# Performance work log

Measured on AMD Instinct MI355X. Metric: run time of the kernel, lower is better.

Reference implementation:

```python
import jax, jax.numpy as jnp
import numpy as np

COUNT_BINS = 8
BOUND = 3.0
MIN_BIN_WIDTH = 1e-3
MIN_BIN_HEIGHT = 1e-3
MIN_DERIVATIVE = 1e-3
EPS = 1e-6


def _made_masks(D, H1, H2, M):
    indeg = np.arange(1, D + 1)                     # input degrees 1..D
    h1 = np.arange(H1) % (D - 1) + 1                # hidden degrees in [1, D-1]
    h2 = np.arange(H2) % (D - 1) + 1
    outdeg = np.tile(indeg, M)                      # (M*D,), reshape-compatible with (M, D)
    m1 = (h1[:, None] >= indeg[None, :]).astype(np.float32)   # (H1, D)
    m2 = (h2[:, None] >= h1[None, :]).astype(np.float32)      # (H2, H1)
    m3 = (outdeg[:, None] > h2[None, :]).astype(np.float32)   # (M*D, H2)
    return jnp.asarray(m1), jnp.asarray(m2), jnp.asarray(m3)


def _rq_spline_forward(x, w, h, d):
    # x: (B, D); w, h: (B, D, K) simplex weights; d: (B, D, K-1) softplus'd interior derivatives
    K = w.shape[-1]
    left, right = -BOUND, BOUND

    widths = MIN_BIN_WIDTH + (1.0 - MIN_BIN_WIDTH * K) * w
    heights = MIN_BIN_HEIGHT + (1.0 - MIN_BIN_HEIGHT * K) * h
    derivs = MIN_DERIVATIVE + d
    ones = jnp.ones_like(derivs[..., :1])
    derivs = jnp.concatenate([ones, derivs, ones], -1)          # (B, D, K+1), boundary slope 1

    cw = jnp.cumsum(widths, -1)
    edge_l = jnp.full_like(cw[..., :1], left)
    edge_r = jnp.full_like(cw[..., :1], right)
    cumw = jnp.concatenate([edge_l, left + (right - left) * cw[..., :-1], edge_r], -1)  # (B, D, K+1)
    widths = cumw[..., 1:] - cumw[..., :-1]
    ch = jnp.cumsum(heights, -1)
    cumh = jnp.concatenate([edge_l, left + (right - left) * ch[..., :-1], edge_r], -1)
    heights = cumh[..., 1:] - cumh[..., :-1]

    inside = (x >= left) & (x <= right)
    xc = jnp.clip(x, left, right)
    # pyro: bin_idx = sum(x >= cumwidths + eps) - 1
    idx = jnp.sum((xc[..., None] >= (cumw + EPS)).astype(jnp.int32), -1) - 1
    idx = jnp.clip(idx, 0, K - 1)                               # (B, D)

    def g(t):
        return jnp.take_along_axis(t, idx[..., None], axis=-1)[..., 0]

    x_k, w_k = g(cumw), g(widths)
    y_k, h_k = g(cumh), g(heights)
    delta = h_k / w_k
    d_k, d_k1 = g(derivs), g(derivs[..., 1:])

    theta = (xc - x_k) / w_k
    tt = theta * (1.0 - theta)
    num = h_k * (delta * theta ** 2 + d_k * tt)
    den = delta + (d_k + d_k1 - 2.0 * delta) * tt
    y = y_k + num / den
    dnum = delta ** 2 * (d_k1 * theta ** 2 + 2.0 * delta * tt + d_k * (1.0 - theta) ** 2)
    ld = jnp.log(dnum) - 2.0 * jnp.log(den)
    return jnp.where(inside, y, x), jnp.where(inside, ld, jnp.zeros_like(ld))


def _forward(x, W1, b1, W2, b2, W3, b3):
    B, D = x.shape
    H1, H2 = W1.shape[0], W2.shape[0]
    K = COUNT_BINS
    M = 3 * K - 1
    m1, m2, m3 = _made_masks(D, H1, H2, M)
    h1 = jax.nn.relu(x @ (W1 * m1).T + b1)
    h2 = jax.nn.relu(h1 @ (W2 * m2).T + b2)
    p = (h2 @ (W3 * m3).T + b3).reshape(B, M, D)                # (B, 3K-1, D)
    w = jax.nn.softmax(jnp.swapaxes(p[:, :K, :], 1, 2), axis=-1)          # (B, D, K)
    hgt = jax.nn.softmax(jnp.swapaxes(p[:, K:2 * K, :], 1, 2), axis=-1)   # (B, D, K)
    d = jax.nn.softplus(jnp.swapaxes(p[:, 2 * K:, :], 1, 2))              # (B, D, K-1)
    z, ld = _rq_spline_forward(x, w, hgt, d)
    return z, ld.sum(-1)


def setup_inputs() -> dict:
    key = jax.random.key(0)
    ks = jax.random.split(key, 7)
    B, D, H1, H2 = 32768, 64, 64, 32
    M = 3 * COUNT_BINS - 1
    s1, s2, s3 = 1.0 / np.sqrt(D), 1.0 / np.sqrt(H1), 1.0 / np.sqrt(H2)
    return {
        "x": jax.random.normal(ks[0], (B, D), jnp.float32),
        "W1": jax.random.uniform(ks[1], (H1, D), jnp.float32, -s1, s1),
        "b1": jax.random.uniform(ks[2], (H1,), jnp.float32, -s1, s1),
        "W2": jax.random.uniform(ks[3], (H2, H1), jnp.float32, -s2, s2),
        "b2": jax.random.uniform(ks[4], (H2,), jnp.float32, -s2, s2),
        "W3": jax.random.uniform(ks[5], (M * D, H2), jnp.float32, -s3, s3),
        "b3": jax.random.uniform(ks[6], (M * D,), jnp.float32, -s3, s3),
    }


def reference(x, W1, b1, W2, b2, W3, b3):
    return _forward(x, W1, b1, W2, b2, W3, b3)
```

## Files before the change

### kernel.cpp

```cpp
#include <hip/hip_runtime.h>

#define NM 23

typedef short short8 __attribute__((ext_vector_type(8)));
typedef float f32x4 __attribute__((ext_vector_type(4)));

#define LOG2E 1.44269504088896340736f

__device__ __forceinline__ float softplus_f(float v) {
  return fmaxf(v, 0.f) + __logf(1.f + __expf(-fabsf(v)));
}

__device__ __forceinline__ float fastrcp(float v) {
  return __builtin_amdgcn_rcpf(v);
}

__device__ __forceinline__ unsigned short bf16_rne(float x) {
  unsigned u = __float_as_uint(x);
  u += 0x7FFFu + ((u >> 16) & 1u);
  return (unsigned short)(u >> 16);
}

__global__ __launch_bounds__(256) void prep_kernel(
    const float* __restrict__ W1, const float* __restrict__ W2,
    const float* __restrict__ W3,
    unsigned short* __restrict__ B1hi,
    unsigned short* __restrict__ B2hi,
    unsigned short* __restrict__ B3hi) {
  const int idx = blockIdx.x * 256 + threadIdx.x;
  const int j = idx & 7, lane = (idx >> 3) & 63;
  const int col = lane & 15, quad = lane >> 4;

  if (idx < 4096) {
    const int rest = idx >> 9, kt = rest & 1, nt = rest >> 1;
    const int k = kt * 32 + quad * 8 + j;
    const int n = nt * 16 + col;
    const float v = ((n % 63) >= k) ? W1[n * 64 + k] : 0.f;
    B1hi[idx] = bf16_rne(v);
  }
  if (idx < 2048) {
    const int rest = idx >> 9, kt = rest & 1, nt = rest >> 1;
    const int k = kt * 32 + quad * 8 + j;
    const int n = nt * 16 + col;
    const float v = ((k % 63) <= n) ? W2[n * 64 + k] : 0.f;
    B2hi[idx] = bf16_rne(v);
  }
  if (idx < 92 * 64 * 8) {
    const int nt = idx >> 9;
    const int n = nt * 16 + col;
    const int d = n & 63;
    const int m = n >> 6;
    const int k = quad * 8 + j;
    float v = (k < d) ? W3[(size_t)n * 32 + k] : 0.f;
    if (m < 16) v *= LOG2E;
    B3hi[idx] = bf16_rne(v);
  }
}

__device__ __forceinline__ short8 cvt_hi(const float* src) {
  const f32x4 a0 = *reinterpret_cast<const f32x4*>(src);
  const f32x4 a1 = *reinterpret_cast<const f32x4*>(src + 4);
  const float af[8] = {a0.x, a0.y, a0.z, a0.w, a1.x, a1.y, a1.z, a1.w};
  short8 hi;
  #pragma unroll
  for (int j = 0; j < 8; ++j) hi[j] = (short)bf16_rne(af[j]);
  return hi;
}

__global__ __launch_bounds__(256, 4) void fused_kernel(
    const float* __restrict__ x,
    const unsigned short* __restrict__ B1hi,
    const float* __restrict__ b1,
    const unsigned short* __restrict__ B2hi,
    const float* __restrict__ b2,
    const unsigned short* __restrict__ B3hi,
    const float* __restrict__ b3,
    float* __restrict__ out, int B) {
  __shared__ float h1s[16][68];
  __shared__ float h2s[16][68];
  __shared__ float b3s[64 * NM];
  __shared__ float ldp[4][16];

  const int t = threadIdx.x;
  const int b0 = blockIdx.x * 16;

  for (int idx = t; idx < 64 * NM; idx += 256) {
    const int dl = idx / NM, m = idx - dl * NM;
    const float s = (m < 16) ? LOG2E : 1.f;
    b3s[idx] = b3[m * 64 + dl] * s;
  }
  __syncthreads();

  const int lane = t & 63;
  const int wv   = __builtin_amdgcn_readfirstlane(t >> 6);
  const int col  = lane & 15;
  const int quad = lane >> 4;

  {
    const int nt1 = wv;
    const float* xrow = x + (size_t)(b0 + col) * 64;
    short8 ah[2];
    #pragma unroll
    for (int kt = 0; kt < 2; ++kt)
      ah[kt] = cvt_hi(xrow + kt * 32 + quad * 8);

    const float bv = b1[nt1 * 16 + col];
    f32x4 acc = {bv, bv, bv, bv};
    #pragma unroll
    for (int kt = 0; kt < 2; ++kt) {
      const size_t off = ((size_t)(nt1 * 2 + kt) * 64 + lane) * 8;
      const short8 bh = *reinterpret_cast<const short8*>(B1hi + off);
      acc = __builtin_amdgcn_mfma_f32_16x16x32_bf16(ah[kt], bh, acc, 0, 0, 0);
    }
    #pragma unroll
    for (int reg = 0; reg < 4; ++reg)
      h1s[quad * 4 + reg][nt1 * 16 + col] = fmaxf(acc[reg], 0.f);
  }
  __syncthreads();

  if (wv < 2) {
    const int nt2 = wv;
    short8 ah[2];
    #pragma unroll
    for (int kt = 0; kt < 2; ++kt)
      ah[kt] = cvt_hi(&h1s[col][kt * 32 + quad * 8]);

    const float bv = b2[nt2 * 16 + col];
    f32x4 acc = {bv, bv, bv, bv};
    #pragma unroll
    for (int kt = 0; kt < 2; ++kt) {
      const size_t off = ((size_t)(nt2 * 2 + kt) * 64 + lane) * 8;
      const short8 bh = *reinterpret_cast<const short8*>(B2hi + off);
      acc = __builtin_amdgcn_mfma_f32_16x16x32_bf16(ah[kt], bh, acc, 0, 0, 0);
    }
    #pragma unroll
    for (int reg = 0; reg < 4; ++reg)
      h2s[quad * 4 + reg][nt2 * 16 + col] = fmaxf(acc[reg], 0.f);
  }
  __syncthreads();

  const int dc = wv;
  const int row0 = quad * 4;
  const int d = dc * 16 + col;

  const short8 ah = cvt_hi(&h2s[col][quad * 8]);

  float xvv[4];
  #pragma unroll
  for (int reg = 0; reg < 4; ++reg)
    xvv[reg] = x[(size_t)(b0 + row0 + reg) * 64 + d];

  __syncthreads();

  float ldr[4] = {0.f, 0.f, 0.f, 0.f};
  const float WSC = 1.0f - 1e-3f * 8.0f;

  float xcv[4], fidx[4], xkv[4], wkv[4], ykv[4], hkv[4];

  {
    f32x4 acc[8];
    #pragma unroll
    for (int m = 0; m < 8; ++m) {
      const float bv = b3s[d * NM + m];
      acc[m] = (f32x4){bv, bv, bv, bv};
    }
    #pragma unroll
    for (int m = 0; m < 8; ++m) {
      const size_t off = ((size_t)(4 * m + dc) * 64 + lane) * 8;
      const short8 bh = *reinterpret_cast<const short8*>(B3hi + off);
      acc[m] = __builtin_amdgcn_mfma_f32_16x16x32_bf16(ah, bh, acc[m], 0, 0, 0);
    }
    #pragma unroll
    for (int reg = 0; reg < 4; ++reg) {
      float ew[8], sw = 0.f;
      #pragma unroll
      for (int k = 0; k < 8; ++k) { ew[k] = exp2f(acc[k][reg]); sw += ew[k]; }
      const float scale = 6.f * WSC * fastrcp(sw);
      float cumw[9];
      cumw[0] = -3.f;
      float prefE = 0.f;
      #pragma unroll
      for (int k = 0; k < 7; ++k) {
        prefE += ew[k];
        const float Ck = -3.f + 6e-3f * (float)(k + 1);
        cumw[k + 1] = fmaf(prefE, scale, Ck);
      }
      cumw[8] = 3.f;

      const float xv = xvv[reg];
      const float xc = fminf(fmaxf(xv, -3.f), 3.f);
      float fi = 0.f, xk = cumw[0], xk1 = cumw[1];
      #pragma unroll
      for (int k = 1; k < 8; ++k) {
        const bool s = xc >= cumw[k] + 1e-6f;
        xk  = s ? cumw[k]     : xk;
        xk1 = s ? cumw[k + 1] : xk1;
        fi  = s ? (float)k    : fi;
      }
      xcv[reg] = xc; fidx[reg] = fi; xkv[reg] = xk; wkv[reg] = xk1 - xk;
    }
  }

  {
    f32x4 acc[8];
    #pragma unroll
    for (int m = 0; m < 8; ++m) {
      const float bv = b3s[d * NM + (8 + m)];
      acc[m] = (f32x4){bv, bv, bv, bv};
    }
    #pragma unroll
    for (int m = 0; m < 8; ++m) {
      const size_t off = ((size_t)(4 * (8 + m) + dc) * 64 + lane) * 8;
      const short8 bh = *reinterpret_cast<const short8*>(B3hi + off);
      acc[m] = __builtin_amdgcn_mfma_f32_16x16x32_bf16(ah, bh, acc[m], 0, 0, 0);
    }
    #pragma unroll
    for (int reg = 0; reg < 4; ++reg) {
      float eh[8], sh = 0.f;
      #pragma unroll
      for (int k = 0; k < 8; ++k) { eh[k] = exp2f(acc[k][reg]); sh += eh[k]; }
      const float scale = 6.f * WSC * fastrcp(sh);
      float cumh[9];
      cumh[0] = -3.f;
      float prefE = 0.f;
      #pragma unroll
      for (int k = 0; k < 7; ++k) {
        prefE += eh[k];
        const float Ck = -3.f + 6e-3f * (float)(k + 1);
        cumh[k + 1] = fmaf(prefE, scale, Ck);
      }
      cumh[8] = 3.f;

      float yk = cumh[0], yk1 = cumh[1];
      #pragma unroll
      for (int k = 1; k < 8; ++k) {
        const bool s = fidx[reg] >= (float)k;
        yk  = s ? cumh[k]     : yk;
        yk1 = s ? cumh[k + 1] : yk1;
      }
      ykv[reg] = yk; hkv[reg] = yk1 - yk;
    }
  }

  {
    f32x4 acc[7];
    #pragma unroll
    for (int m = 0; m < 7; ++m) {
      const float bv = b3s[d * NM + (16 + m)];
      acc[m] = (f32x4){bv, bv, bv, bv};
    }
    #pragma unroll
    for (int m = 0; m < 7; ++m) {
      const size_t off = ((size_t)(4 * (16 + m) + dc) * 64 + lane) * 8;
      const short8 bh = *reinterpret_cast<const short8*>(B3hi + off);
      acc[m] = __builtin_amdgcn_mfma_f32_16x16x32_bf16(ah, bh, acc[m], 0, 0, 0);
    }
    #pragma unroll
    for (int reg = 0; reg < 4; ++reg) {
      float p[7];
      #pragma unroll
      for (int k = 0; k < 7; ++k) p[k] = acc[k][reg];
      const float fi = fidx[reg];

      float pa = p[0], pb = p[0];
      #pragma unroll
      for (int k = 2; k < 8; ++k) pa = (fi >= (float)k) ? p[k - 1] : pa;
      #pragma unroll
      for (int k = 1; k < 7; ++k) pb = (fi >= (float)k) ? p[k] : pb;
      const float spa = 1e-3f + softplus_f(pa);
      const float spb = 1e-3f + softplus_f(pb);
      const float dk  = (fi >= 0.5f) ? spa : 1.f;
      const float dk1 = (fi >= 6.5f) ? 1.f : spb;

      const float xc = xcv[reg], xk = xkv[reg], wk = wkv[reg];
      const float yk = ykv[reg], hk = hkv[reg];
      const float invwk = fastrcp(wk);
      const float delta = hk * invwk;
      const float theta = (xc - xk) * invwk;
      const float omt = 1.f - theta;
      const float tt = theta * omt;
      const float th2 = theta * theta;
      const float num = hk * (delta * th2 + dk * tt);
      const float den = delta + (dk + dk1 - 2.f * delta) * tt;
      const float rden = fastrcp(den);
      const float yv = yk + num * rden;
      const float dnum =
          delta * delta * (dk1 * th2 + 2.f * delta * tt + dk * omt * omt);
      const float ldv = __logf(dnum * rden * rden);

      const float xv = xvv[reg];
      const bool inside = (xv >= -3.f) && (xv <= 3.f);
      h2s[row0 + reg][d] = inside ? yv : xv;
      ldr[reg] += inside ? ldv : 0.f;
    }
  }

  #pragma unroll
  for (int mask = 1; mask <= 8; mask <<= 1) {
    #pragma unroll
    for (int reg = 0; reg < 4; ++reg)
      ldr[reg] += __shfl_xor(ldr[reg], mask, 64);
  }
  if (col == 0) {
    #pragma unroll
    for (int reg = 0; reg < 4; ++reg)
      ldp[dc][row0 + reg] = ldr[reg];
  }

  __syncthreads();

  if (t < 16)
    out[(size_t)B * 64 + b0 + t] =
        (ldp[0][t] + ldp[1][t]) + (ldp[2][t] + ldp[3][t]);

  {
    const int rr = t >> 4, c4 = (t & 15) * 4;
    const float4 v = make_float4(h2s[rr][c4 + 0], h2s[rr][c4 + 1],
                                 h2s[rr][c4 + 2], h2s[rr][c4 + 3]);
    *reinterpret_cast<float4*>(out + (size_t)(b0 + rr) * 64 + c4) = v;
  }
}

extern "C" void kernel_launch(void* const* d_in, const int* in_sizes, int n_in,
                              void* d_out, int out_size, void* d_ws, size_t ws_size,
                              hipStream_t stream) {
  const float* x  = (const float*)d_in[0];
  const float* W1 = (const float*)d_in[1];
  const float* b1 = (const float*)d_in[2];
  const float* W2 = (const float*)d_in[3];
  const float* b2 = (const float*)d_in[4];
  const float* W3 = (const float*)d_in[5];
  const float* b3 = (const float*)d_in[6];
  float* out = (float*)d_out;
  char* ws   = (char*)d_ws;

  unsigned short* B1hi = (unsigned short*)(ws);
  unsigned short* B2hi = (unsigned short*)(ws + 8192);
  unsigned short* B3hi = (unsigned short*)(ws + 16384);

  const int B = in_sizes[0] / 64;

  prep_kernel<<<184, 256, 0, stream>>>(W1, W2, W3, B1hi, B2hi, B3hi);

  fused_kernel<<<B / 16, 256, 0, stream>>>(
      x, B1hi, b1, B2hi, b2, B3hi, b3, out, B);
}
```

Measured before the change: 103.5 us.

## Recompute MLP hidden layers per wave to eliminate block barriers

Each wave now computes all of layers 1 and 2 redundantly into its own shared-memory slice instead of splitting the tiles across waves. This removes the block-wide barriers between the layers and before the spline stage, and lets each wave write its own output columns directly. In exchange, the layer-1 and layer-2 MFMA work and weight loads are duplicated four times and shared memory per block grows.

```diff
diff --git a/kernel.cpp b/kernel.cpp
--- a/kernel.cpp
+++ b/kernel.cpp
@@ -76,8 +76,7 @@
     const unsigned short* __restrict__ B3hi,
     const float* __restrict__ b3,
     float* __restrict__ out, int B) {
-  __shared__ float h1s[16][68];
-  __shared__ float h2s[16][68];
+  __shared__ float slc[4][16][68];
   __shared__ float b3s[64 * NM];
   __shared__ float ldp[4][16];
 
@@ -95,62 +94,63 @@
   const int wv   = __builtin_amdgcn_readfirstlane(t >> 6);
   const int col  = lane & 15;
   const int quad = lane >> 4;
-
-  {
-    const int nt1 = wv;
+  float (*my)[68] = slc[wv];
+
+  {
     const float* xrow = x + (size_t)(b0 + col) * 64;
     short8 ah[2];
     #pragma unroll
     for (int kt = 0; kt < 2; ++kt)
       ah[kt] = cvt_hi(xrow + kt * 32 + quad * 8);
 
-    const float bv = b1[nt1 * 16 + col];
-    f32x4 acc = {bv, bv, bv, bv};
-    #pragma unroll
-    for (int kt = 0; kt < 2; ++kt) {
-      const size_t off = ((size_t)(nt1 * 2 + kt) * 64 + lane) * 8;
-      const short8 bh = *reinterpret_cast<const short8*>(B1hi + off);
-      acc = __builtin_amdgcn_mfma_f32_16x16x32_bf16(ah[kt], bh, acc, 0, 0, 0);
-    }
-    #pragma unroll
-    for (int reg = 0; reg < 4; ++reg)
-      h1s[quad * 4 + reg][nt1 * 16 + col] = fmaxf(acc[reg], 0.f);
-  }
-  __syncthreads();
-
-  if (wv < 2) {
-    const int nt2 = wv;
+    #pragma unroll
+    for (int nt = 0; nt < 4; ++nt) {
+      const float bv = b1[nt * 16 + col];
+      f32x4 acc = {bv, bv, bv, bv};
+      #pragma unroll
+      for (int kt = 0; kt < 2; ++kt) {
+        const size_t off = ((size_t)(nt * 2 + kt) * 64 + lane) * 8;
+        const short8 bh = *reinterpret_cast<const short8*>(B1hi + off);
+        acc = __builtin_amdgcn_mfma_f32_16x16x32_bf16(ah[kt], bh, acc, 0, 0, 0);
+      }
+      #pragma unroll
+      for (int reg = 0; reg < 4; ++reg)
+        my[quad * 4 + reg][nt * 16 + col] = fmaxf(acc[reg], 0.f);
+    }
+  }
+
+  {
     short8 ah[2];
     #pragma unroll
     for (int kt = 0; kt < 2; ++kt)
-      ah[kt] = cvt_hi(&h1s[col][kt * 32 + quad * 8]);
-
-    const float bv = b2[nt2 * 16 + col];
-    f32x4 acc = {bv, bv, bv, bv};
-    #pragma unroll
-    for (int kt = 0; kt < 2; ++kt) {
-      const size_t off = ((size_t)(nt2 * 2 + kt) * 64 + lane) * 8;
-      const short8 bh = *reinterpret_cast<const short8*>(B2hi + off);
-      acc = __builtin_amdgcn_mfma_f32_16x16x32_bf16(ah[kt], bh, acc, 0, 0, 0);
-    }
-    #pragma unroll
-    for (int reg = 0; reg < 4; ++reg)
-      h2s[quad * 4 + reg][nt2 * 16 + col] = fmaxf(acc[reg], 0.f);
-  }
-  __syncthreads();
+      ah[kt] = cvt_hi(&my[col][kt * 32 + quad * 8]);
+
+    #pragma unroll
+    for (int nt = 0; nt < 2; ++nt) {
+      const float bv = b2[nt * 16 + col];
+      f32x4 acc = {bv, bv, bv, bv};
+      #pragma unroll
+      for (int kt = 0; kt < 2; ++kt) {
+        const size_t off = ((size_t)(nt * 2 + kt) * 64 + lane) * 8;
+        const short8 bh = *reinterpret_cast<const short8*>(B2hi + off);
+        acc = __builtin_amdgcn_mfma_f32_16x16x32_bf16(ah[kt], bh, acc, 0, 0, 0);
+      }
+      #pragma unroll
+      for (int reg = 0; reg < 4; ++reg)
+        my[quad * 4 + reg][nt * 16 + col] = fmaxf(acc[reg], 0.f);
+    }
+  }
 
   const int dc = wv;
   const int row0 = quad * 4;
   const int d = dc * 16 + col;
 
-  const short8 ah = cvt_hi(&h2s[col][quad * 8]);
+  const short8 ah = cvt_hi(&my[col][quad * 8]);
 
   float xvv[4];
   #pragma unroll
   for (int reg = 0; reg < 4; ++reg)
     xvv[reg] = x[(size_t)(b0 + row0 + reg) * 64 + d];
-
-  __syncthreads();
 
   float ldr[4] = {0.f, 0.f, 0.f, 0.f};
   const float WSC = 1.0f - 1e-3f * 8.0f;
@@ -290,7 +290,7 @@
 
       const float xv = xvv[reg];
       const bool inside = (xv >= -3.f) && (xv <= 3.f);
-      h2s[row0 + reg][d] = inside ? yv : xv;
+      my[row0 + reg][d] = inside ? yv : xv;
       ldr[reg] += inside ? ldv : 0.f;
     }
   }
@@ -305,6 +305,16 @@
     #pragma unroll
     for (int reg = 0; reg < 4; ++reg)
       ldp[dc][row0 + reg] = ldr[reg];
+  }
+
+  {
+    const int rr = lane >> 2, ci = (lane & 3) * 4;
+    const float4 v = make_float4(my[rr][dc * 16 + ci + 0],
+                                 my[rr][dc * 16 + ci + 1],
+                                 my[rr][dc * 16 + ci + 2],
+                                 my[rr][dc * 16 + ci + 3]);
+    *reinterpret_cast<float4*>(
+        out + (size_t)(b0 + rr) * 64 + dc * 16 + ci) = v;
   }
 
   __syncthreads();
@@ -312,13 +322,6 @@
   if (t < 16)
     out[(size_t)B * 64 + b0 + t] =
         (ldp[0][t] + ldp[1][t]) + (ldp[2][t] + ldp[3][t]);
-
-  {
-    const int rr = t >> 4, c4 = (t & 15) * 4;
-    const float4 v = make_float4(h2s[rr][c4 + 0], h2s[rr][c4 + 1],
-                                 h2s[rr][c4 + 2], h2s[rr][c4 + 3]);
-    *reinterpret_cast<float4*>(out + (size_t)(b0 + rr) * 64 + c4) = v;
-  }
 }
 
 extern "C" void kernel_launch(void* const* d_in, const int* in_sizes, int n_in,
```

After: 108.1 us. 1.04x slower.
